# Performance work log

Measured on AMD Instinct MI355X. Metric: run time of the kernel, lower is better.

Reference implementation:

```python
import jax, jax.numpy as jnp
import numpy as np

N_NODES = 50000
N_EDGES = 800000
IN_F = 128
OUT_F = 128
HEADS = 8
HEAD_DIM = OUT_F // HEADS
EDGE_F = 32


def setup_inputs() -> dict:
    key = jax.random.key(0)
    ks = jax.random.split(key, 14)
    s = lambda fan_in: 1.0 / np.sqrt(fan_in)
    return {
        "node_features": jax.random.normal(ks[0], (N_NODES, IN_F), jnp.float32),
        "edge_index": jax.random.randint(ks[1], (2, N_EDGES), 0, N_NODES, jnp.int64),
        "edge_features": jax.random.normal(ks[2], (N_EDGES, EDGE_F), jnp.float32),
        "Wq": jax.random.uniform(ks[3], (IN_F, OUT_F), jnp.float32, -s(IN_F), s(IN_F)),
        "bq": jnp.zeros((OUT_F,), jnp.float32),
        "Wk": jax.random.uniform(ks[4], (IN_F, OUT_F), jnp.float32, -s(IN_F), s(IN_F)),
        "bk": jnp.zeros((OUT_F,), jnp.float32),
        "Wv": jax.random.uniform(ks[5], (IN_F, OUT_F), jnp.float32, -s(IN_F), s(IN_F)),
        "bv": jnp.zeros((OUT_F,), jnp.float32),
        "We": jax.random.uniform(ks[6], (EDGE_F, HEADS), jnp.float32, -s(EDGE_F), s(EDGE_F)),
        "be": jnp.zeros((HEADS,), jnp.float32),
        "Wo": jax.random.uniform(ks[7], (OUT_F, OUT_F), jnp.float32, -s(OUT_F), s(OUT_F)),
        "bo": jnp.zeros((OUT_F,), jnp.float32),
    }


def reference(node_features, edge_index, edge_features,
              Wq, bq, Wk, bk, Wv, bv, We, be, Wo, bo):
    n_nodes = node_features.shape[0]
    n_edges = edge_index.shape[1]
    sources, targets = edge_index[0], edge_index[1]
    scale = HEAD_DIM ** -0.5

    # dense projections: [n_nodes, heads, head_dim]
    Q = (node_features @ Wq + bq).reshape(n_nodes, HEADS, HEAD_DIM)
    K = (node_features @ Wk + bk).reshape(n_nodes, HEADS, HEAD_DIM)
    V = (node_features @ Wv + bv).reshape(n_nodes, HEADS, HEAD_DIM)

    # gather by edge
    Q_t = Q[targets]           # [n_edges, heads, head_dim]
    K_s = K[sources]
    V_s = V[sources]

    scores = jnp.sum(Q_t * K_s, axis=-1) * scale      # [n_edges, heads]
    scores = scores + (edge_features @ We + be)       # edge bias

    # segment softmax over incoming edges of each target node
    max_s = jax.ops.segment_max(scores, targets, num_segments=n_nodes)
    scores = scores - max_s[targets]
    exp_s = jnp.exp(scores)
    denom = jax.ops.segment_sum(exp_s, targets, num_segments=n_nodes) + 1e-10
    probs = exp_s / denom[targets]                    # [n_edges, heads]

    weighted_V = probs[:, :, None] * V_s              # [n_edges, heads, head_dim]
    aggregated = jax.ops.segment_sum(
        weighted_V.reshape(n_edges, -1), targets, num_segments=n_nodes)
    return aggregated @ Wo + bo
```

## Files before the change

### kernel.cpp

```cpp
#include <hip/hip_runtime.h>

typedef __attribute__((ext_vector_type(8))) short shortx8;
typedef __attribute__((ext_vector_type(4))) float floatx4;
typedef unsigned short u16;
typedef unsigned int u32;

__device__ __forceinline__ float bf2f(unsigned short u) {
    union { unsigned int i; float f; } v; v.i = ((unsigned int)u) << 16; return v.f;
}
__device__ __forceinline__ float bfl(u32 u) {
    union { u32 i; float f; } v; v.i = u << 16; return v.f;
}
__device__ __forceinline__ float bfh(u32 u) {
    union { u32 i; float f; } v; v.i = u & 0xFFFF0000u; return v.f;
}
__device__ __forceinline__ unsigned short f2bf(float f) {
    union { float f; unsigned int i; } v; v.f = f;
    unsigned int x = v.i;
    unsigned int r = x + 0x7FFFu + ((x >> 16) & 1u);
    return (unsigned short)(r >> 16);
}
__device__ __forceinline__ u32 pack2bf(float a, float b) {
    return (u32)f2bf(a) | ((u32)f2bf(b) << 16);
}
__device__ __forceinline__ float ldf(const void* p, int i, bool f32) {
    return f32 ? ((const float*)p)[i] : bf2f(((const u16*)p)[i]);
}

__global__ __launch_bounds__(256) void prep_all_k(
    const u16* __restrict__ nf, const int* __restrict__ ei,
    const void* __restrict__ W0, const void* __restrict__ W1,
    const void* __restrict__ W2, const void* __restrict__ W3,
    const void* __restrict__ b0, const void* __restrict__ b1,
    const void* __restrict__ b2, const void* __restrict__ b3,
    const void* __restrict__ We, const void* __restrict__ be,
    int* __restrict__ flags, int* __restrict__ deg,
    u16* __restrict__ WT, float* __restrict__ biasWs,
    float* __restrict__ WeWs, float* __restrict__ beWs, int M)
{
    int tid = threadIdx.x;
    int bid = blockIdx.x;
    if (bid >= 33) {
        int i = (bid - 33) * 256 + tid;
        if (i < M) deg[i] = 0;
        return;
    }
    __shared__ int cnt[2];
    if (tid < 2) cnt[tid] = 0;
    __syncthreads();
    int c0 = 0;
    for (int i = tid; i < 8192; i += 256) {
        u16 v = nf[i];
        if ((v & 0x7F80u) == 0x7F80u) c0++;
    }
    atomicAdd(&cnt[0], c0);
    if (bid == 32) {
        int c1 = 0;
        for (int i = tid; i < 1024; i += 256) {
            if (ei[2 * i + 1] != 0) c1++;
        }
        atomicAdd(&cnt[1], c1);
    }
    __syncthreads();
    bool f32 = cnt[0] > 6;

    if (bid < 32) {
        int t = bid * 256 + tid;
        int mat  = t >> 11;
        int r    = t & 2047;
        int lane = r & 63;
        int ks   = (r >> 6) & 3;
        int ct   = r >> 8;
        const void* W = (mat == 0) ? W0 : (mat == 1) ? W1 : (mat == 2) ? W2 : W3;
        int k0  = ks * 32 + (lane >> 4) * 8;
        int col = ct * 16 + (lane & 15);
        u16 tmp[8];
#pragma unroll
        for (int j = 0; j < 8; ++j) {
            int off = (k0 + j) * 128 + col;
            tmp[j] = f32 ? f2bf(((const float*)W)[off]) : ((const u16*)W)[off];
        }
        *(shortx8*)(WT + (size_t)t * 8) = *(const shortx8*)tmp;
    } else {
        if (tid == 0) {
            flags[0] = f32 ? 1 : 0;
            flags[1] = (cnt[1] < 100) ? 1 : 0;
        }
        if (tid < 128) {
            biasWs[0 * 128 + tid] = ldf(b0, tid, f32);
            biasWs[1 * 128 + tid] = ldf(b1, tid, f32);
            biasWs[2 * 128 + tid] = ldf(b2, tid, f32);
            biasWs[3 * 128 + tid] = ldf(b3, tid, f32);
        }
        WeWs[tid] = ldf(We, tid, f32);
        if (tid < 8) beWs[tid] = ldf(be, tid, f32);
    }
}

__global__ __launch_bounds__(256) void hist_k(
    const int* __restrict__ ei, int* __restrict__ deg,
    int E, const int* __restrict__ flags)
{
    int e = blockIdx.x * 256 + threadIdx.x;
    if (e >= E) return;
    int tgt = flags[1] ? ei[2 * (E + e)] : ei[E + e];
    atomicAdd(&deg[tgt], 1);
}

__global__ __launch_bounds__(256) void scan1_k(
    const int* __restrict__ deg, int* __restrict__ incl, int* __restrict__ bsum, int M)
{
    __shared__ int s[256];
    int tid = threadIdx.x;
    int i = blockIdx.x * 256 + tid;
    int v = (i < M) ? deg[i] : 0;
    s[tid] = v;
    __syncthreads();
#pragma unroll
    for (int off = 1; off < 256; off <<= 1) {
        int t = (tid >= off) ? s[tid - off] : 0;
        __syncthreads();
        s[tid] += t;
        __syncthreads();
    }
    if (i < M) incl[i] = s[tid];
    if (tid == 255) bsum[blockIdx.x] = s[255];
}

__global__ __launch_bounds__(256) void scan23_k(
    const int* __restrict__ bsum, int* __restrict__ incl_cur,
    const int* __restrict__ deg, int* __restrict__ rowptr, int M, int nb)
{
    __shared__ int s[256];
    int tid = threadIdx.x;
    int v = (tid < nb) ? bsum[tid] : 0;
    s[tid] = v;
    __syncthreads();
#pragma unroll
    for (int off = 1; off < 256; off <<= 1) {
        int t = (tid >= off) ? s[tid - off] : 0;
        __syncthreads();
        s[tid] += t;
        __syncthreads();
    }
    int b = blockIdx.x;
    int boffb = (b == 0) ? 0 : s[b - 1];
    int i = b * 256 + tid;
    if (i >= M) return;
    int r = incl_cur[i] + boffb;
    rowptr[i + 1] = r;
    incl_cur[i] = r - deg[i];
    if (i == 0) rowptr[0] = 0;
}

__global__ __launch_bounds__(256) void qkv_scatter_k(
    const void* __restrict__ A, int M,
    const u16* __restrict__ WT, const float* __restrict__ biasWs,
    u16* __restrict__ Qb, u16* __restrict__ KVb,
    const int* __restrict__ ei, const void* __restrict__ ef,
    int* __restrict__ cur,
    const float* __restrict__ WeWs, const float* __restrict__ beWs,
    uint4* __restrict__ rec, int E,
    const int* __restrict__ flags, int gblocks)
{
    __shared__ float sWe[256];
    __shared__ float sbe[8];

    if (blockIdx.x < gblocks) {
        bool aF32 = flags[0] != 0;
        int lane = threadIdx.x & 63;
        int wave = threadIdx.x >> 6;
        int quad = lane >> 4;
        int l15  = lane & 15;
        int m0   = blockIdx.x * 128 + wave * 32;

        shortx8 afrag[2][4];
#pragma unroll
        for (int mt = 0; mt < 2; ++mt) {
            int row = m0 + mt * 16 + l15;
            row = row < M ? row : M - 1;
#pragma unroll
            for (int ks = 0; ks < 4; ++ks) {
                size_t base = (size_t)row * 128 + ks * 32 + quad * 8;
                if (aF32) {
                    const floatx4* ap = (const floatx4*)((const float*)A + base);
                    floatx4 f0 = ap[0], f1 = ap[1];
                    u16 tmp[8];
#pragma unroll
                    for (int j = 0; j < 4; ++j) { tmp[j] = f2bf(f0[j]); tmp[4 + j] = f2bf(f1[j]); }
                    afrag[mt][ks] = *(const shortx8*)tmp;
                } else {
                    afrag[mt][ks] = *(const shortx8*)((const u16*)A + base);
                }
            }
        }

#pragma unroll
        for (int mat = 0; mat < 3; ++mat) {
            floatx4 acc[2][8];
#pragma unroll
            for (int a = 0; a < 2; ++a)
#pragma unroll
                for (int b = 0; b < 8; ++b)
                    acc[a][b] = (floatx4){0.f, 0.f, 0.f, 0.f};
#pragma unroll
            for (int ks = 0; ks < 4; ++ks) {
#pragma unroll
                for (int ct = 0; ct < 8; ++ct) {
                    shortx8 bfrag = *(const shortx8*)(WT + (size_t)mat * 16384 +
                                                      ((size_t)(ct * 4 + ks) * 64 + lane) * 8);
                    acc[0][ct] = __builtin_amdgcn_mfma_f32_16x16x32_bf16(afrag[0][ks], bfrag, acc[0][ct], 0, 0, 0);
                    acc[1][ct] = __builtin_amdgcn_mfma_f32_16x16x32_bf16(afrag[1][ks], bfrag, acc[1][ct], 0, 0, 0);
                }
            }
            u16* base = (mat == 0) ? Qb : (mat == 1) ? KVb : (KVb + 128);
            int stride = (mat == 0) ? 128 : 256;
#pragma unroll
            for (int ct = 0; ct < 8; ++ct) {
                int col = ct * 16 + l15;
                float bs = biasWs[mat * 128 + col];
#pragma unroll
                for (int mt = 0; mt < 2; ++mt) {
#pragma unroll
                    for (int r = 0; r < 4; ++r) {
                        int row = m0 + mt * 16 + quad * 4 + r;
                        if (row < M)
                            base[(size_t)row * stride + col] = f2bf(acc[mt][ct][r] + bs);
                    }
                }
            }
        }
    } else {
        int tid = threadIdx.x;
        sWe[tid] = WeWs[tid];
        if (tid < 8) sbe[tid] = beWs[tid];
        __syncthreads();

        int e = (blockIdx.x - gblocks) * 256 + tid;
        if (e >= E) return;
        bool f32 = flags[0] != 0;
        bool i64 = flags[1] != 0;

        int src = i64 ? ei[2 * e]       : ei[e];
        int tgt = i64 ? ei[2 * (E + e)] : ei[E + e];
        int pos = atomicAdd(&cur[tgt], 1);

        float v[32];
        if (f32) {
            const floatx4* ep = (const floatx4*)((const float*)ef + (size_t)e * 32);
#pragma unroll
            for (int g = 0; g < 8; ++g) {
                floatx4 t = ep[g];
#pragma unroll
                for (int j = 0; j < 4; ++j) v[g * 4 + j] = t[j];
            }
        } else {
            const shortx8* ep = (const shortx8*)((const u16*)ef + (size_t)e * 32);
#pragma unroll
            for (int g = 0; g < 4; ++g) {
                shortx8 t = ep[g];
#pragma unroll
                for (int j = 0; j < 8; ++j) v[g * 8 + j] = bf2f((unsigned short)t[j]);
            }
        }
        float eb[8];
#pragma unroll
        for (int h = 0; h < 8; ++h) eb[h] = sbe[h];
#pragma unroll
        for (int k = 0; k < 32; ++k)
#pragma unroll
            for (int h = 0; h < 8; ++h) eb[h] += v[k] * sWe[k * 8 + h];

        uint4 r0, r1;
        r0.x = (u32)src;
        r0.y = pack2bf(eb[0], eb[1]);
        r0.z = pack2bf(eb[2], eb[3]);
        r0.w = pack2bf(eb[4], eb[5]);
        r1.x = pack2bf(eb[6], eb[7]);
        r1.y = 0; r1.z = 0; r1.w = 0;
        rec[(size_t)pos * 2]     = r0;
        rec[(size_t)pos * 2 + 1] = r1;
    }
}

__global__ __launch_bounds__(256) void node_agg_k(
    const uint4* __restrict__ rec, const int* __restrict__ rowptr,
    const u16* __restrict__ Qb, const u16* __restrict__ KVb,
    u16* __restrict__ aggN, int M, int E)
{
    int wave = threadIdx.x >> 6;
    int lane = threadIdx.x & 63;
    int n = blockIdx.x * 4 + wave;
    if (n >= M) return;
    int g = lane >> 4;
    int w = lane & 15;
    int h = w >> 1;

    int beg = rowptr[n], end = rowptr[n + 1];
    int ridx = beg + (lane >> 1);
    if (ridx >= E) ridx = E - 1;
    uint4 pv = rec[(size_t)ridx * 2 + (lane & 1)];

    uint4 qw = ((const uint4*)(Qb + (size_t)n * 128))[w];
    float q0 = bfl(qw.x), q1 = bfh(qw.x), q2 = bfl(qw.y), q3 = bfh(qw.y);
    float q4 = bfl(qw.z), q5 = bfh(qw.z), q6 = bfl(qw.w), q7 = bfh(qw.w);

    float acc[8];
#pragma unroll
    for (int j = 0; j < 8; ++j) acc[j] = 0.f;
    float dsum = 0.f;

    for (int i = beg; i < end; i += 8) {
        int idxA = i + g;
        int idxB = i + 4 + g;
        bool vA = idxA < end;
        bool vB = idxB < end;
        int cA = vA ? idxA : (end - 1);
        int cB = vB ? idxB : (end - 1);
        int offA = cA - beg;
        int offB = cB - beg;

        int srcA, srcB;
        float ebA, ebB;
        if (offA < 32) {
            srcA = __shfl((int)pv.x, 2 * offA);
            u32 w01 = __shfl((int)pv.y, 2 * offA);
            u32 w23 = __shfl((int)pv.z, 2 * offA);
            u32 w45 = __shfl((int)pv.w, 2 * offA);
            u32 w67 = __shfl((int)pv.x, 2 * offA + 1);
            u32 sel = (h < 2) ? w01 : (h < 4) ? w23 : (h < 6) ? w45 : w67;
            ebA = (h & 1) ? bfh(sel) : bfl(sel);
        } else {
            const u32* rw = (const u32*)(rec + (size_t)cA * 2);
            srcA = (int)rw[0];
            u32 sel = rw[1 + h / 2];
            ebA = (h & 1) ? bfh(sel) : bfl(sel);
        }
        if (offB < 32) {
            srcB = __shfl((int)pv.x, 2 * offB);
            u32 w01 = __shfl((int)pv.y, 2 * offB);
            u32 w23 = __shfl((int)pv.z, 2 * offB);
            u32 w45 = __shfl((int)pv.w, 2 * offB);
            u32 w67 = __shfl((int)pv.x, 2 * offB + 1);
            u32 sel = (h < 2) ? w01 : (h < 4) ? w23 : (h < 6) ? w45 : w67;
            ebB = (h & 1) ? bfh(sel) : bfl(sel);
        } else {
            const u32* rw = (const u32*)(rec + (size_t)cB * 2);
            srcB = (int)rw[0];
            u32 sel = rw[1 + h / 2];
            ebB = (h & 1) ? bfh(sel) : bfl(sel);
        }

        const uint4* kpA = (const uint4*)(KVb + (size_t)srcA * 256);
        const uint4* kpB = (const uint4*)(KVb + (size_t)srcB * 256);
        uint4 kwA = kpA[w];
        uint4 kwB = kpB[w];
        uint4 vwA = kpA[16 + w];
        uint4 vwB = kpB[16 + w];

        float partA = q0 * bfl(kwA.x) + q1 * bfh(kwA.x)
                    + q2 * bfl(kwA.y) + q3 * bfh(kwA.y)
                    + q4 * bfl(kwA.z) + q5 * bfh(kwA.z)
                    + q6 * bfl(kwA.w) + q7 * bfh(kwA.w);
        float partB = q0 * bfl(kwB.x) + q1 * bfh(kwB.x)
                    + q2 * bfl(kwB.y) + q3 * bfh(kwB.y)
                    + q4 * bfl(kwB.z) + q5 * bfh(kwB.z)
                    + q6 * bfl(kwB.w) + q7 * bfh(kwB.w);
        partA += __shfl_xor(partA, 1);
        partB += __shfl_xor(partB, 1);
        float pA = vA ? __expf(partA * 0.25f + ebA) : 0.f;
        float pB = vB ? __expf(partB * 0.25f + ebB) : 0.f;
        dsum += pA + pB;
        acc[0] += pA * bfl(vwA.x) + pB * bfl(vwB.x);
        acc[1] += pA * bfh(vwA.x) + pB * bfh(vwB.x);
        acc[2] += pA * bfl(vwA.y) + pB * bfl(vwB.y);
        acc[3] += pA * bfh(vwA.y) + pB * bfh(vwB.y);
        acc[4] += pA * bfl(vwA.z) + pB * bfl(vwB.z);
        acc[5] += pA * bfh(vwA.z) + pB * bfh(vwB.z);
        acc[6] += pA * bfl(vwA.w) + pB * bfl(vwB.w);
        acc[7] += pA * bfh(vwA.w) + pB * bfh(vwB.w);
    }

    dsum += __shfl_xor(dsum, 16);
    dsum += __shfl_xor(dsum, 32);
#pragma unroll
    for (int j = 0; j < 8; ++j) {
        acc[j] += __shfl_xor(acc[j], 16);
        acc[j] += __shfl_xor(acc[j], 32);
    }
    if (g == 0) {
        float inv = 1.0f / (dsum + 1e-10f);
        uint4 o;
        o.x = (u32)f2bf(acc[0] * inv) | ((u32)f2bf(acc[1] * inv) << 16);
        o.y = (u32)f2bf(acc[2] * inv) | ((u32)f2bf(acc[3] * inv) << 16);
        o.z = (u32)f2bf(acc[4] * inv) | ((u32)f2bf(acc[5] * inv) << 16);
        o.w = (u32)f2bf(acc[6] * inv) | ((u32)f2bf(acc[7] * inv) << 16);
        ((uint4*)(aggN + (size_t)n * 128))[w] = o;
    }
}

__global__ __launch_bounds__(256) void out_gemm_k(
    const u16* __restrict__ A, int M,
    const u16* __restrict__ WT, const float* __restrict__ bias,
    void* __restrict__ out, const int* __restrict__ flags)
{
    bool oF32 = flags[0] != 0;
    int lane = threadIdx.x & 63;
    int wave = threadIdx.x >> 6;
    int quad = lane >> 4;
    int l15  = lane & 15;
    int m0   = blockIdx.x * 128 + wave * 32;

    floatx4 acc[2][8];
#pragma unroll
    for (int a = 0; a < 2; ++a)
#pragma unroll
        for (int b = 0; b < 8; ++b)
            acc[a][b] = (floatx4){0.f, 0.f, 0.f, 0.f};

#pragma unroll
    for (int ks = 0; ks < 4; ++ks) {
        shortx8 afrag[2];
#pragma unroll
        for (int mt = 0; mt < 2; ++mt) {
            int row = m0 + mt * 16 + l15;
            row = row < M ? row : M - 1;
            afrag[mt] = *(const shortx8*)(A + (size_t)row * 128 + ks * 32 + quad * 8);
        }
#pragma unroll
        for (int ct = 0; ct < 8; ++ct) {
            shortx8 bfrag = *(const shortx8*)(WT + ((size_t)(ct * 4 + ks) * 64 + lane) * 8);
            acc[0][ct] = __builtin_amdgcn_mfma_f32_16x16x32_bf16(afrag[0], bfrag, acc[0][ct], 0, 0, 0);
            acc[1][ct] = __builtin_amdgcn_mfma_f32_16x16x32_bf16(afrag[1], bfrag, acc[1][ct], 0, 0, 0);
        }
    }

#pragma unroll
    for (int ct = 0; ct < 8; ++ct) {
        int col = ct * 16 + l15;
        float bs = bias[col];
#pragma unroll
        for (int mt = 0; mt < 2; ++mt) {
#pragma unroll
            for (int r = 0; r < 4; ++r) {
                int row = m0 + mt * 16 + quad * 4 + r;
                if (row < M) {
                    float v = acc[mt][ct][r] + bs;
                    if (oF32) ((float*)out)[(size_t)row * 128 + col] = v;
                    else      ((u16*)out)[(size_t)row * 128 + col] = f2bf(v);
                }
            }
        }
    }
}

extern "C" void kernel_launch(void* const* d_in, const int* in_sizes, int n_in,
                              void* d_out, int out_size, void* d_ws, size_t ws_size,
                              hipStream_t stream)
{
    const void* nf = d_in[0];
    const int*  ei = (const int*)d_in[1];
    const void* ef = d_in[2];
    const void* Wq = d_in[3];  const void* bq = d_in[4];
    const void* Wk = d_in[5];  const void* bk = d_in[6];
    const void* Wv = d_in[7];  const void* bv = d_in[8];
    const void* We = d_in[9];  const void* be = d_in[10];
    const void* Wo = d_in[11]; const void* bo = d_in[12];

    int M = in_sizes[0] / 128;
    int E = in_sizes[1] / 2;
    int nb = (M + 255) / 256;

    char* ws = (char*)d_ws;
    int*   flags  = (int*)(ws + 0);
    float* biasWs = (float*)(ws + 256);
    float* WeWs   = (float*)(ws + 2304);
    float* beWs   = (float*)(ws + 3328);
    u16*   WT     = (u16*)(ws + 4096);
    size_t O1 = 4096 + 131072;
    size_t qrow  = (size_t)M * 128 * 2;
    size_t kvrow = (size_t)M * 256 * 2;
    u16* Qb  = (u16*)(ws + O1);
    u16* KVb = (u16*)(ws + O1 + qrow);
    size_t O2 = O1 + qrow + kvrow;
    uint4* rec = (uint4*)(ws + O2);
    size_t O3 = O2 + (size_t)E * 32;
    int* deg    = (int*)(ws + O3);
    int* incl   = deg + M;
    int* rowptr = incl + M;
    int* bsum   = rowptr + M + 1;
    u16* aggN   = Qb;

    prep_all_k<<<33 + nb, 256, 0, stream>>>((const u16*)nf, ei,
                                            Wq, Wk, Wv, Wo, bq, bk, bv, bo, We, be,
                                            flags, deg, WT, biasWs, WeWs, beWs, M);

    int eblocks = (E + 255) / 256;
    hist_k<<<eblocks, 256, 0, stream>>>(ei, deg, E, flags);
    scan1_k<<<nb, 256, 0, stream>>>(deg, incl, bsum, M);
    scan23_k<<<nb, 256, 0, stream>>>(bsum, incl, deg, rowptr, M, nb);

    int gblocks = (M + 127) / 128;
    qkv_scatter_k<<<gblocks + eblocks, 256, 0, stream>>>(
        nf, M, WT, biasWs, Qb, KVb,
        ei, ef, incl , WeWs, beWs, rec, E, flags, gblocks);

    node_agg_k<<<(M + 3) / 4, 256, 0, stream>>>(rec, rowptr, Qb, KVb, aggN, M, E);

    out_gemm_k<<<gblocks, 256, 0, stream>>>(aggN, M, WT + 3 * 16384, biasWs + 384, d_out, flags);
}
```

Measured before the change: 383.6 us.

## Record per-edge rank in histogram pass and split fused GEMM/scatter kernel

```diff
diff --git a/kernel.cpp b/kernel.cpp
--- a/kernel.cpp
+++ b/kernel.cpp
@@ -97,14 +97,14 @@
     }
 }
 
-__global__ __launch_bounds__(256) void hist_k(
-    const int* __restrict__ ei, int* __restrict__ deg,
+__global__ __launch_bounds__(256) void hist_rank_k(
+    const int* __restrict__ ei, int* __restrict__ deg, int* __restrict__ rank,
     int E, const int* __restrict__ flags)
 {
     int e = blockIdx.x * 256 + threadIdx.x;
     if (e >= E) return;
     int tgt = flags[1] ? ei[2 * (E + e)] : ei[E + e];
-    atomicAdd(&deg[tgt], 1);
+    rank[e] = atomicAdd(&deg[tgt], 1);
 }
 
 __global__ __launch_bounds__(256) void scan1_k(
@@ -128,8 +128,8 @@
 }
 
 __global__ __launch_bounds__(256) void scan23_k(
-    const int* __restrict__ bsum, int* __restrict__ incl_cur,
-    const int* __restrict__ deg, int* __restrict__ rowptr, int M, int nb)
+    const int* __restrict__ bsum, const int* __restrict__ incl,
+    int* __restrict__ rowptr, int M, int nb)
 {
     __shared__ int s[256];
     int tid = threadIdx.x;
@@ -147,140 +147,138 @@
     int boffb = (b == 0) ? 0 : s[b - 1];
     int i = b * 256 + tid;
     if (i >= M) return;
-    int r = incl_cur[i] + boffb;
-    rowptr[i + 1] = r;
-    incl_cur[i] = r - deg[i];
+    rowptr[i + 1] = incl[i] + boffb;
     if (i == 0) rowptr[0] = 0;
 }
 
-__global__ __launch_bounds__(256) void qkv_scatter_k(
+__global__ __launch_bounds__(256) void qkv_gemm_k(
     const void* __restrict__ A, int M,
     const u16* __restrict__ WT, const float* __restrict__ biasWs,
     u16* __restrict__ Qb, u16* __restrict__ KVb,
+    const int* __restrict__ flags)
+{
+    bool aF32 = flags[0] != 0;
+    int lane = threadIdx.x & 63;
+    int wave = threadIdx.x >> 6;
+    int quad = lane >> 4;
+    int l15  = lane & 15;
+    int m0   = blockIdx.x * 128 + wave * 32;
+
+    shortx8 afrag[2][4];
+#pragma unroll
+    for (int mt = 0; mt < 2; ++mt) {
+        int row = m0 + mt * 16 + l15;
+        row = row < M ? row : M - 1;
+#pragma unroll
+        for (int ks = 0; ks < 4; ++ks) {
+            size_t base = (size_t)row * 128 + ks * 32 + quad * 8;
+            if (aF32) {
+                const floatx4* ap = (const floatx4*)((const float*)A + base);
+                floatx4 f0 = ap[0], f1 = ap[1];
+                u16 tmp[8];
+#pragma unroll
+                for (int j = 0; j < 4; ++j) { tmp[j] = f2bf(f0[j]); tmp[4 + j] = f2bf(f1[j]); }
+                afrag[mt][ks] = *(const shortx8*)tmp;
+            } else {
+                afrag[mt][ks] = *(const shortx8*)((const u16*)A + base);
+            }
+        }
+    }
+
+#pragma unroll
+    for (int mat = 0; mat < 3; ++mat) {
+        floatx4 acc[2][8];
+#pragma unroll
+        for (int a = 0; a < 2; ++a)
+#pragma unroll
+            for (int b = 0; b < 8; ++b)
+                acc[a][b] = (floatx4){0.f, 0.f, 0.f, 0.f};
+#pragma unroll
+        for (int ks = 0; ks < 4; ++ks) {
+#pragma unroll
+            for (int ct = 0; ct < 8; ++ct) {
+                shortx8 bfrag = *(const shortx8*)(WT + (size_t)mat * 16384 +
+                                                  ((size_t)(ct * 4 + ks) * 64 + lane) * 8);
+                acc[0][ct] = __builtin_amdgcn_mfma_f32_16x16x32_bf16(afrag[0][ks], bfrag, acc[0][ct], 0, 0, 0);
+                acc[1][ct] = __builtin_amdgcn_mfma_f32_16x16x32_bf16(afrag[1][ks], bfrag, acc[1][ct], 0, 0, 0);
+            }
+        }
+        u16* base = (mat == 0) ? Qb : (mat == 1) ? KVb : (KVb + 128);
+        int stride = (mat == 0) ? 128 : 256;
+#pragma unroll
+        for (int ct = 0; ct < 8; ++ct) {
+            int col = ct * 16 + l15;
+            float bs = biasWs[mat * 128 + col];
+#pragma unroll
+            for (int mt = 0; mt < 2; ++mt) {
+#pragma unroll
+                for (int r = 0; r < 4; ++r) {
+                    int row = m0 + mt * 16 + quad * 4 + r;
+                    if (row < M)
+                        base[(size_t)row * stride + col] = f2bf(acc[mt][ct][r] + bs);
+                }
+            }
+        }
+    }
+}
+
+__global__ __launch_bounds__(256) void scatter_eb_k(
     const int* __restrict__ ei, const void* __restrict__ ef,
-    int* __restrict__ cur,
+    const int* __restrict__ rank, const int* __restrict__ rowptr,
     const float* __restrict__ WeWs, const float* __restrict__ beWs,
-    uint4* __restrict__ rec, int E,
-    const int* __restrict__ flags, int gblocks)
+    uint4* __restrict__ rec, int E, const int* __restrict__ flags)
 {
     __shared__ float sWe[256];
     __shared__ float sbe[8];
-
-    if (blockIdx.x < gblocks) {
-        bool aF32 = flags[0] != 0;
-        int lane = threadIdx.x & 63;
-        int wave = threadIdx.x >> 6;
-        int quad = lane >> 4;
-        int l15  = lane & 15;
-        int m0   = blockIdx.x * 128 + wave * 32;
-
-        shortx8 afrag[2][4];
-#pragma unroll
-        for (int mt = 0; mt < 2; ++mt) {
-            int row = m0 + mt * 16 + l15;
-            row = row < M ? row : M - 1;
-#pragma unroll
-            for (int ks = 0; ks < 4; ++ks) {
-                size_t base = (size_t)row * 128 + ks * 32 + quad * 8;
-                if (aF32) {
-                    const floatx4* ap = (const floatx4*)((const float*)A + base);
-                    floatx4 f0 = ap[0], f1 = ap[1];
-                    u16 tmp[8];
-#pragma unroll
-                    for (int j = 0; j < 4; ++j) { tmp[j] = f2bf(f0[j]); tmp[4 + j] = f2bf(f1[j]); }
-                    afrag[mt][ks] = *(const shortx8*)tmp;
-                } else {
-                    afrag[mt][ks] = *(const shortx8*)((const u16*)A + base);
-                }
-            }
-        }
-
-#pragma unroll
-        for (int mat = 0; mat < 3; ++mat) {
-            floatx4 acc[2][8];
-#pragma unroll
-            for (int a = 0; a < 2; ++a)
-#pragma unroll
-                for (int b = 0; b < 8; ++b)
-                    acc[a][b] = (floatx4){0.f, 0.f, 0.f, 0.f};
-#pragma unroll
-            for (int ks = 0; ks < 4; ++ks) {
-#pragma unroll
-                for (int ct = 0; ct < 8; ++ct) {
-                    shortx8 bfrag = *(const shortx8*)(WT + (size_t)mat * 16384 +
-                                                      ((size_t)(ct * 4 + ks) * 64 + lane) * 8);
-                    acc[0][ct] = __builtin_amdgcn_mfma_f32_16x16x32_bf16(afrag[0][ks], bfrag, acc[0][ct], 0, 0, 0);
-                    acc[1][ct] = __builtin_amdgcn_mfma_f32_16x16x32_bf16(afrag[1][ks], bfrag, acc[1][ct], 0, 0, 0);
-                }
-            }
-            u16* base = (mat == 0) ? Qb : (mat == 1) ? KVb : (KVb + 128);
-            int stride = (mat == 0) ? 128 : 256;
-#pragma unroll
-            for (int ct = 0; ct < 8; ++ct) {
-                int col = ct * 16 + l15;
-                float bs = biasWs[mat * 128 + col];
-#pragma unroll
-                for (int mt = 0; mt < 2; ++mt) {
-#pragma unroll
-                    for (int r = 0; r < 4; ++r) {
-                        int row = m0 + mt * 16 + quad * 4 + r;
-                        if (row < M)
-                            base[(size_t)row * stride + col] = f2bf(acc[mt][ct][r] + bs);
-                    }
-                }
-            }
+    int tid = threadIdx.x;
+    sWe[tid] = WeWs[tid];
+    if (tid < 8) sbe[tid] = beWs[tid];
+    __syncthreads();
+
+    int e = blockIdx.x * 256 + tid;
+    if (e >= E) return;
+    bool f32 = flags[0] != 0;
+    bool i64 = flags[1] != 0;
+
+    int src = i64 ? ei[2 * e]       : ei[e];
+    int tgt = i64 ? ei[2 * (E + e)] : ei[E + e];
+    int pos = rowptr[tgt] + rank[e];
+
+    float v[32];
+    if (f32) {
+        const floatx4* ep = (const floatx4*)((const float*)ef + (size_t)e * 32);
+#pragma unroll
+        for (int g = 0; g < 8; ++g) {
+            floatx4 t = ep[g];
+#pragma unroll
+            for (int j = 0; j < 4; ++j) v[g * 4 + j] = t[j];
         }
     } else {
-        int tid = threadIdx.x;
-        sWe[tid] = WeWs[tid];
-        if (tid < 8) sbe[tid] = beWs[tid];
-        __syncthreads();
-
-        int e = (blockIdx.x - gblocks) * 256 + tid;
-        if (e >= E) return;
-        bool f32 = flags[0] != 0;
-        bool i64 = flags[1] != 0;
-
-        int src = i64 ? ei[2 * e]       : ei[e];
-        int tgt = i64 ? ei[2 * (E + e)] : ei[E + e];
-        int pos = atomicAdd(&cur[tgt], 1);
-
-        float v[32];
-        if (f32) {
-            const floatx4* ep = (const floatx4*)((const float*)ef + (size_t)e * 32);
-#pragma unroll
-            for (int g = 0; g < 8; ++g) {
-                floatx4 t = ep[g];
-#pragma unroll
-                for (int j = 0; j < 4; ++j) v[g * 4 + j] = t[j];
-            }
-        } else {
-            const shortx8* ep = (const shortx8*)((const u16*)ef + (size_t)e * 32);
-#pragma unroll
-            for (int g = 0; g < 4; ++g) {
-                shortx8 t = ep[g];
-#pragma unroll
-                for (int j = 0; j < 8; ++j) v[g * 8 + j] = bf2f((unsigned short)t[j]);
-            }
-        }
-        float eb[8];
-#pragma unroll
-        for (int h = 0; h < 8; ++h) eb[h] = sbe[h];
-#pragma unroll
-        for (int k = 0; k < 32; ++k)
-#pragma unroll
-            for (int h = 0; h < 8; ++h) eb[h] += v[k] * sWe[k * 8 + h];
-
-        uint4 r0, r1;
-        r0.x = (u32)src;
-        r0.y = pack2bf(eb[0], eb[1]);
-        r0.z = pack2bf(eb[2], eb[3]);
-        r0.w = pack2bf(eb[4], eb[5]);
-        r1.x = pack2bf(eb[6], eb[7]);
-        r1.y = 0; r1.z = 0; r1.w = 0;
-        rec[(size_t)pos * 2]     = r0;
-        rec[(size_t)pos * 2 + 1] = r1;
-    }
+        const shortx8* ep = (const shortx8*)((const u16*)ef + (size_t)e * 32);
+#pragma unroll
+        for (int g = 0; g < 4; ++g) {
+            shortx8 t = ep[g];
+#pragma unroll
+            for (int j = 0; j < 8; ++j) v[g * 8 + j] = bf2f((unsigned short)t[j]);
+        }
+    }
+    float eb[8];
+#pragma unroll
+    for (int h = 0; h < 8; ++h) eb[h] = sbe[h];
+#pragma unroll
+    for (int k = 0; k < 32; ++k)
+#pragma unroll
+        for (int h = 0; h < 8; ++h) eb[h] += v[k] * sWe[k * 8 + h];
+
+    uint4 r0, r1;
+    r0.x = (u32)src;
+    r0.y = pack2bf(eb[0], eb[1]);
+    r0.z = pack2bf(eb[2], eb[3]);
+    r0.w = pack2bf(eb[4], eb[5]);
+    r1.x = pack2bf(eb[6], eb[7]);
+    r1.y = 0; r1.z = 0; r1.w = 0;
+    rec[(size_t)pos * 2]     = r0;
+    rec[(size_t)pos * 2 + 1] = r1;
 }
 
 __global__ __launch_bounds__(256) void node_agg_k(
@@ -485,7 +483,8 @@
     size_t O2 = O1 + qrow + kvrow;
     uint4* rec = (uint4*)(ws + O2);
     size_t O3 = O2 + (size_t)E * 32;
-    int* deg    = (int*)(ws + O3);
+    int* rank   = (int*)(ws + O3);
+    int* deg    = rank + E;
     int* incl   = deg + M;
     int* rowptr = incl + M;
     int* bsum   = rowptr + M + 1;
@@ -496,14 +495,15 @@
                                             flags, deg, WT, biasWs, WeWs, beWs, M);
 
     int eblocks = (E + 255) / 256;
-    hist_k<<<eblocks, 256, 0, stream>>>(ei, deg, E, flags);
+    hist_rank_k<<<eblocks, 256, 0, stream>>>(ei, deg, rank, E, flags);
     scan1_k<<<nb, 256, 0, stream>>>(deg, incl, bsum, M);
-    scan23_k<<<nb, 256, 0, stream>>>(bsum, incl, deg, rowptr, M, nb);
+    scan23_k<<<nb, 256, 0, stream>>>(bsum, incl, rowptr, M, nb);
 
     int gblocks = (M + 127) / 128;
-    qkv_scatter_k<<<gblocks + eblocks, 256, 0, stream>>>(
-        nf, M, WT, biasWs, Qb, KVb,
-        ei, ef, incl , WeWs, beWs, rec, E, flags, gblocks);
+    qkv_gemm_k<<<gblocks, 256, 0, stream>>>(nf, M, WT, biasWs, Qb, KVb, flags);
+
+    scatter_eb_k<<<eblocks, 256, 0, stream>>>(ei, ef, rank, rowptr, WeWs, beWs,
+                                              rec, E, flags);
 
     node_agg_k<<<(M + 3) / 4, 256, 0, stream>>>(rec, rowptr, Qb, KVb, aggN, M, E);
 
```

Measured after the change: 391.9 us. 1.02x slower.
